# Optimization experiments

Hardware: AMD Instinct MI355X
Metric: run time of the kernel (lower is better)

The kernel has to match this reference:

```python
import jax, jax.numpy as jnp
import numpy as np


def setup_inputs() -> dict:
    key = jax.random.key(0)
    k1, k2, k3, k4 = jax.random.split(key, 4)
    B, A, E, K, H = 256, 64, 128, 6, 256
    return {
        "bond_representations": jax.random.normal(k1, (1, B, E, H), dtype=jnp.float32),
        "bond_pairs": jax.random.randint(k2, (B, E, 2), 0, A, dtype=jnp.int32),
        "bond_neighbors": jax.random.randint(k3, (B, E, K), 0, E, dtype=jnp.int32),
        "xyz": jax.random.normal(k4, (B, A, 3), dtype=jnp.float32),
    }


def _distance_weight(xyz, bond_pairs):
    # xyz: [B, A, 3]; bond_pairs: [B, E, 2] -> gathered [B, E, 2, 3]
    d = jax.vmap(lambda x, p: x[p])(xyz, bond_pairs)
    diff = d[:, :, 0, :] - d[:, :, 1, :]          # [B, E, 3]
    d2 = jnp.sum(diff * diff, axis=-1)            # [B, E]
    inv = 1.0 / d2                                # squared-distance reciprocal weight
    return jnp.where(jnp.isinf(inv), jnp.zeros_like(inv), inv)


def reference(bond_representations, bond_pairs, bond_neighbors, xyz):
    # include_3d=True, mean_readout=False (sum readout)
    dist = _distance_weight(xyz, bond_pairs)                       # [B, E]
    weighted = dist[None, :, :, None] * bond_representations      # [1, B, E, H]
    wb = weighted[0]                                               # [B, E, H]
    # gather neighbor bond features: [B, E, K, H], then sum over K
    nbf = jax.vmap(lambda w, nb: w[nb])(wb, bond_neighbors)
    msg = jnp.sum(nbf, axis=2)                                     # [B, E, H]
    return msg[None]                                               # [1, B, E, H]
```

## Files before the change

### kernel.cpp

```cpp
#include <hip/hip_runtime.h>
#include <math.h>

#define NB 256
#define NA 64
#define NE 128
#define NK 6
#define NH 256

__global__ __launch_bounds__(256, 1) void edge_msg_kernel(
    const float* __restrict__ rep,
    const int*   __restrict__ pairs,
    const int*   __restrict__ nbrs,
    const float* __restrict__ xyz,
    float*       __restrict__ out)
{
    extern __shared__ float smem[];
    float* s_rep = smem;
    float* s_w   = smem + NE * NH;
    int*   s_nb  = (int*)(s_w + NE);

    const int b   = blockIdx.x;
    const int tid = threadIdx.x;

    const int* nbr_b = nbrs + b * NE * NK;
#pragma unroll
    for (int i = tid; i < NE * NK; i += 256) s_nb[i] = nbr_b[i];

    if (tid < NE) {
        const int p0 = pairs[(b * NE + tid) * 2 + 0];
        const int p1 = pairs[(b * NE + tid) * 2 + 1];
        const float* x0 = xyz + ((size_t)b * NA + p0) * 3;
        const float* x1 = xyz + ((size_t)b * NA + p1) * 3;
        const float dx = x0[0] - x1[0];
        const float dy = x0[1] - x1[1];
        const float dz = x0[2] - x1[2];
        const float d2 = dx * dx + dy * dy + dz * dz;
        float inv = 1.0f / d2;
        if (isinf(inv)) inv = 0.0f;
        s_w[tid] = inv;
    }

    const float4* g4 = (const float4*)(rep + (size_t)b * NE * NH);
    float4*       l4 = (float4*)s_rep;
#pragma unroll
    for (int i = 0; i < 32; i += 8) {
        float4 r[8];
#pragma unroll
        for (int j = 0; j < 8; ++j) r[j] = g4[tid + (i + j) * 256];
#pragma unroll
        for (int j = 0; j < 8; ++j) l4[tid + (i + j) * 256] = r[j];
    }
    __syncthreads();

    const int wid  = tid >> 6;
    const int lane = tid & 63;
    const float4* lrep4 = (const float4*)s_rep;
    float4* outb = (float4*)(out + (size_t)b * NE * NH);

#pragma unroll 4
    for (int ei = 0; ei < 32; ++ei) {
        const int e = wid * 32 + ei;
        float4 acc = make_float4(0.f, 0.f, 0.f, 0.f);
#pragma unroll
        for (int k = 0; k < NK; ++k) {
            const int   nb = s_nb[e * NK + k];
            const float w  = s_w[nb];
            const float4 v = lrep4[nb * (NH / 4) + lane];
            acc.x += w * v.x;
            acc.y += w * v.y;
            acc.z += w * v.z;
            acc.w += w * v.w;
        }
        outb[e * (NH / 4) + lane] = acc;
    }
}

extern "C" void kernel_launch(void* const* d_in, const int* in_sizes, int n_in,
                              void* d_out, int out_size, void* d_ws, size_t ws_size,
                              hipStream_t stream) {
    const float* rep   = (const float*)d_in[0];
    const int*   pairs = (const int*)  d_in[1];
    const int*   nbrs  = (const int*)  d_in[2];
    const float* xyz   = (const float*)d_in[3];
    float*       out   = (float*)d_out;

    const size_t lds_bytes = (size_t)(NE * NH + NE) * sizeof(float)
                           + (size_t)(NE * NK) * sizeof(int);
    edge_msg_kernel<<<dim3(NB), dim3(256), lds_bytes, stream>>>(rep, pairs, nbrs, xyz, out);
}
```

Measured before the change: 93.79 us.

## Split each batch across 8 workgroups and gather neighbor rows from global memory

New measurement: 95.59 us. Within noise of the previous version (+1.9%).

```diff
diff --git a/kernel.cpp b/kernel.cpp
--- a/kernel.cpp
+++ b/kernel.cpp
@@ -7,24 +7,27 @@
 #define NK 6
 #define NH 256
 
-__global__ __launch_bounds__(256, 1) void edge_msg_kernel(
+#define EPB 16
+#define BLOCKS_PER_B (NE / EPB)
+#define NWG (NB * BLOCKS_PER_B)
+
+__global__ __launch_bounds__(256, 4) void edge_msg_kernel(
     const float* __restrict__ rep,
     const int*   __restrict__ pairs,
     const int*   __restrict__ nbrs,
     const float* __restrict__ xyz,
     float*       __restrict__ out)
 {
-    extern __shared__ float smem[];
-    float* s_rep = smem;
-    float* s_w   = smem + NE * NH;
-    int*   s_nb  = (int*)(s_w + NE);
+    __shared__ float s_w[NE];
+    __shared__ int   s_nb[EPB * NK];
 
-    const int b   = blockIdx.x;
+    const int p       = blockIdx.x;
+    const int logical = (p & 7) * (NWG / 8) + (p >> 3);
+    const int b       = logical >> 3;
+    const int chunk   = logical & (BLOCKS_PER_B - 1);
+    const int e0      = chunk * EPB;
+
     const int tid = threadIdx.x;
-
-    const int* nbr_b = nbrs + b * NE * NK;
-#pragma unroll
-    for (int i = tid; i < NE * NK; i += 256) s_nb[i] = nbr_b[i];
 
     if (tid < NE) {
         const int p0 = pairs[(b * NE + tid) * 2 + 0];
@@ -40,38 +43,32 @@
         s_w[tid] = inv;
     }
 
-    const float4* g4 = (const float4*)(rep + (size_t)b * NE * NH);
-    float4*       l4 = (float4*)s_rep;
-#pragma unroll
-    for (int i = 0; i < 32; i += 8) {
-        float4 r[8];
-#pragma unroll
-        for (int j = 0; j < 8; ++j) r[j] = g4[tid + (i + j) * 256];
-#pragma unroll
-        for (int j = 0; j < 8; ++j) l4[tid + (i + j) * 256] = r[j];
+    if (tid < EPB * NK) {
+        s_nb[tid] = nbrs[((size_t)b * NE + e0) * NK + tid];
     }
     __syncthreads();
 
     const int wid  = tid >> 6;
     const int lane = tid & 63;
-    const float4* lrep4 = (const float4*)s_rep;
-    float4* outb = (float4*)(out + (size_t)b * NE * NH);
 
-#pragma unroll 4
-    for (int ei = 0; ei < 32; ++ei) {
-        const int e = wid * 32 + ei;
+    const float4* rep4 = (const float4*)(rep + (size_t)b * NE * NH);
+    float4*       out4 = (float4*)(out + (size_t)b * NE * NH);
+
+#pragma unroll
+    for (int ei = 0; ei < EPB / 4; ++ei) {
+        const int e = wid * (EPB / 4) + ei;
         float4 acc = make_float4(0.f, 0.f, 0.f, 0.f);
 #pragma unroll
         for (int k = 0; k < NK; ++k) {
             const int   nb = s_nb[e * NK + k];
             const float w  = s_w[nb];
-            const float4 v = lrep4[nb * (NH / 4) + lane];
+            const float4 v = rep4[nb * (NH / 4) + lane];
             acc.x += w * v.x;
             acc.y += w * v.y;
             acc.z += w * v.z;
             acc.w += w * v.w;
         }
-        outb[e * (NH / 4) + lane] = acc;
+        out4[(size_t)(e0 + e) * (NH / 4) + lane] = acc;
     }
 }
 
@@ -84,7 +81,5 @@
     const float* xyz   = (const float*)d_in[3];
     float*       out   = (float*)d_out;
 
-    const size_t lds_bytes = (size_t)(NE * NH + NE) * sizeof(float)
-                           + (size_t)(NE * NK) * sizeof(int);
-    edge_msg_kernel<<<dim3(NB), dim3(256), lds_bytes, stream>>>(rep, pairs, nbrs, xyz, out);
+    edge_msg_kernel<<<dim3(NWG), dim3(256), 0, stream>>>(rep, pairs, nbrs, xyz, out);
 }
```
